# Optimization experiments

Measured on AMD Instinct MI355X. Metric: run time of the kernel, lower is better.

## Reference

```python
import jax, jax.numpy as jnp
import numpy as np

N = 50000      # nodes
E = 800000     # edges (avg degree 16)
IN = 256       # in_feats
H = 128        # hidden_feats
C = 40         # out_feats == num classes (label dim)
LPA_ITERS = 10


def setup_inputs() -> dict:
    key = jax.random.key(0)
    ks = jax.random.split(key, 9)
    features = jax.random.normal(ks[0], (N, IN), dtype=jnp.float32)
    labels = jax.random.normal(ks[1], (N, C), dtype=jnp.float32)
    mask = jax.random.randint(ks[2], (N,), 0, 2) > 0          # bool [N]
    src = jax.random.randint(ks[3], (E,), 0, N, dtype=jnp.int32)
    dst = jax.random.randint(ks[4], (E,), 0, N, dtype=jnp.int32)
    W1 = jax.random.normal(ks[5], (IN, H), dtype=jnp.float32) * (1.0 / np.sqrt(IN))
    b1 = jnp.zeros((H,), dtype=jnp.float32)
    W2 = jax.random.normal(ks[6], (H, C), dtype=jnp.float32) * (1.0 / np.sqrt(H))
    b2 = jnp.zeros((C,), dtype=jnp.float32)
    return {"features": features, "labels": labels, "mask": mask,
            "src": src, "dst": dst, "W1": W1, "b1": b1, "W2": W2, "b2": b2}


def reference(features, labels, mask, src, dst, W1, b1, W2, b2):
    ones_e = jnp.ones((E,), dtype=jnp.float32)
    deg_out = jax.ops.segment_sum(ones_e, src, num_segments=N)  # out-degree
    deg_in = jax.ops.segment_sum(ones_e, dst, num_segments=N)   # in-degree
    norm_src = jnp.maximum(deg_out, 1.0) ** -0.5                 # DGL clamps deg>=1
    norm_dst = jnp.maximum(deg_in, 1.0) ** -0.5

    def gconv(x, W, b):
        # DGL GraphConv, norm='both': D_in^{-1/2} A^T D_out^{-1/2} (x W) + b
        h = (x @ W) * norm_src[:, None]                          # [N, d_out]
        agg = jax.ops.segment_sum(h[src], dst, num_segments=N)   # gather+scatter-add
        return agg * norm_dst[:, None] + b

    x = jax.nn.relu(gconv(features, W1, b1))
    # dropout identity in eval mode
    x = gconv(x, W2, b2)

    # Label propagation: adj[src,dst]=1 so (adj @ y)[i] = sum_{(i->j)} y[j]
    masked_labels = jnp.where(mask[:, None], labels, 0.0)

    def step(y, _):
        y = jax.ops.segment_sum(y[dst], src, num_segments=N)
        y = jnp.where(mask[:, None], labels, y)
        return y, None

    y, _ = jax.lax.scan(step, masked_labels, None, length=LPA_ITERS)
    return x, y
```

## Files before the change

### kernel.cpp

```cpp
#include <hip/hip_runtime.h>

#define Nn 50000
#define Ee 800000
#define INF_ 256
#define HID 128
#define NC 40
#define CAPD 48
#define CAPS 48
#define LPA_ITERS 10
#define NB 98
#define BSH 9
#define EPB 2048
#define NBLK ((Ee + EPB - 1) / EPB)
#define CAPB_D 10240
#define CAPB_S 6144

typedef __attribute__((ext_vector_type(8))) short bfrag;
typedef __attribute__((ext_vector_type(4))) float ffrag;

__device__ inline unsigned f2bf2(float a, float b) {
    unsigned ua = __float_as_uint(a); ua += 0x7FFFu + ((ua >> 16) & 1u);
    unsigned ub = __float_as_uint(b); ub += 0x7FFFu + ((ub >> 16) & 1u);
    return (ua >> 16) | (ub & 0xFFFF0000u);
}
__device__ inline unsigned short f2bf(float a) {
    unsigned ua = __float_as_uint(a); ua += 0x7FFFu + ((ua >> 16) & 1u);
    return (unsigned short)(ua >> 16);
}
__device__ inline float bf_lo(unsigned u) { return __uint_as_float(u << 16); }
__device__ inline float bf_hi(unsigned u) { return __uint_as_float(u & 0xFFFF0000u); }

__global__ void detect_fmt(const unsigned int* __restrict__ m, int* flag) {
    int i = blockIdx.x * blockDim.x + threadIdx.x;
    if (i < 12500) {
        if (m[i] > 1u) atomicOr(flag, 1);
    }
}

__device__ inline bool read_mask(const void* mask, int node, int fmt) {
    if (fmt) return ((const unsigned char*)mask)[node] != 0;
    return ((const int*)mask)[node] != 0;
}

__global__ __launch_bounds__(256) void bin_edges(
    const int* __restrict__ src, const int* __restrict__ dst,
    const void* __restrict__ mask, const int* __restrict__ flag,
    int* __restrict__ cnt_src,
    int* __restrict__ cur_d, int* __restrict__ cur_s,
    unsigned* __restrict__ bkt_d, unsigned* __restrict__ bkt_s) {
    __shared__ unsigned stage_d[EPB];
    __shared__ unsigned stage_s[EPB];
    __shared__ int hd[NB], od[NB + 1], cd[NB], gd_[NB];
    __shared__ int hs[NB], os_[NB + 1], cs_[NB], gs_[NB];
    int tid = threadIdx.x;
    int e0 = blockIdx.x * EPB;
    int fmt = *flag;
    if (tid < NB) { hd[tid] = 0; hs[tid] = 0; }
    __syncthreads();

    int rs[EPB / 256], rd[EPB / 256];
    unsigned um = 0;
#pragma unroll
    for (int k = 0; k < EPB / 256; k++) {
        int e = e0 + tid + k * 256;
        rs[k] = -1; rd[k] = -1;
        if (e < Ee) {
            int s = src[e], d = dst[e];
            rs[k] = s; rd[k] = d;
            atomicAdd(&cnt_src[s], 1);
            atomicAdd(&hd[d >> BSH], 1);
            if (!read_mask(mask, s, fmt)) {
                um |= (1u << k);
                atomicAdd(&hs[s >> BSH], 1);
            }
        }
    }
    __syncthreads();
    if (tid == 0) {
        int run = 0;
        for (int b = 0; b < NB; b++) { od[b] = run; run += hd[b]; }
        od[NB] = run;
        run = 0;
        for (int b = 0; b < NB; b++) { os_[b] = run; run += hs[b]; }
        os_[NB] = run;
    }
    __syncthreads();
    if (tid < NB) {
        gd_[tid] = hd[tid] ? atomicAdd(&cur_d[tid], hd[tid]) : 0;
        gs_[tid] = hs[tid] ? atomicAdd(&cur_s[tid], hs[tid]) : 0;
        cd[tid] = od[tid];
        cs_[tid] = os_[tid];
    }
    __syncthreads();
#pragma unroll
    for (int k = 0; k < EPB / 256; k++) {
        if (rd[k] >= 0) {
            int p = atomicAdd(&cd[rd[k] >> BSH], 1);
            stage_d[p] = ((unsigned)rd[k] << 16) | (unsigned)rs[k];
            if (um & (1u << k)) {
                int q = atomicAdd(&cs_[rs[k] >> BSH], 1);
                stage_s[q] = ((unsigned)rs[k] << 16) | (unsigned)rd[k];
            }
        }
    }
    __syncthreads();
    int totd = od[NB];
    for (int i = tid; i < totd; i += 256) {
        int lo = 0, hi = NB;
        while (hi - lo > 1) {
            int mid = (lo + hi) >> 1;
            if (od[mid] <= i) lo = mid; else hi = mid;
        }
        int pos = gd_[lo] + (i - od[lo]);
        if (pos < CAPB_D) bkt_d[(size_t)lo * CAPB_D + pos] = stage_d[i];
    }
    int tots = os_[NB];
    for (int i = tid; i < tots; i += 256) {
        int lo = 0, hi = NB;
        while (hi - lo > 1) {
            int mid = (lo + hi) >> 1;
            if (os_[mid] <= i) lo = mid; else hi = mid;
        }
        int pos = gs_[lo] + (i - os_[lo]);
        if (pos < CAPB_S) bkt_s[(size_t)lo * CAPB_S + pos] = stage_s[i];
    }
}

__global__ __launch_bounds__(256) void build_csr_dst(
    const unsigned* __restrict__ bkt, const int* __restrict__ cur,
    int* __restrict__ adj, int* __restrict__ cnt) {
    __shared__ int lc[512];
    int b = blockIdx.x, tid = threadIdx.x;
    lc[tid] = 0; lc[tid + 256] = 0;
    __syncthreads();
    int n = cur[b]; if (n > CAPB_D) n = CAPB_D;
    int n0 = b << BSH;
    const unsigned* base = bkt + (size_t)b * CAPB_D;
    for (int i = tid; i < n; i += 256) {
        unsigned r = base[i];
        int d = r >> 16, s = r & 0xffff;
        int sl = atomicAdd(&lc[d - n0], 1);
        if (sl < CAPD) adj[d * CAPD + sl] = s;
    }
    __syncthreads();
    int g0 = n0 + tid;
    if (g0 < Nn) cnt[g0] = lc[tid];
    g0 += 256;
    if (g0 < Nn) cnt[g0] = lc[tid + 256];
}

__global__ __launch_bounds__(256) void build_csr_src(
    const unsigned* __restrict__ bkt, const int* __restrict__ cur,
    const void* __restrict__ mask, const int* __restrict__ flag,
    int* __restrict__ adj, int* __restrict__ cnt_u, int* __restrict__ cnt_m) {
    __shared__ int lu[512], lm[512];
    int b = blockIdx.x, tid = threadIdx.x;
    lu[tid] = 0; lu[tid + 256] = 0; lm[tid] = 0; lm[tid + 256] = 0;
    __syncthreads();
    int fmt = *flag;
    int n = cur[b]; if (n > CAPB_S) n = CAPB_S;
    int n0 = b << BSH;
    const unsigned* base = bkt + (size_t)b * CAPB_S;
    for (int i = tid; i < n; i += 256) {
        unsigned r = base[i];
        int s = r >> 16, d = r & 0xffff;
        if (read_mask(mask, d, fmt)) {
            int sl = atomicAdd(&lm[s - n0], 1);
            if (sl < CAPS) adj[s * CAPS + (CAPS - 1 - sl)] = d;
        } else {
            int sl = atomicAdd(&lu[s - n0], 1);
            if (sl < CAPS) adj[s * CAPS + sl] = d;
        }
    }
    __syncthreads();
    int g0 = n0 + tid;
    if (g0 < Nn) { cnt_u[g0] = lu[tid]; cnt_m[g0] = lm[tid]; }
    g0 += 256;
    if (g0 < Nn) { cnt_u[g0] = lu[tid + 256]; cnt_m[g0] = lm[tid + 256]; }
}

__global__ void build_unmasked(const void* __restrict__ mask,
                               const int* __restrict__ flag,
                               int* n_un, int* __restrict__ ulist) {
    int i = blockIdx.x * blockDim.x + threadIdx.x;
    if (i < Nn) {
        if (!read_mask(mask, i, *flag)) {
            int p = atomicAdd(n_un, 1);
            ulist[p] = i;
        }
    }
}

__global__ void prep_w1t(const float* __restrict__ W1,
                         unsigned short* __restrict__ W1t) {
    int c = blockIdx.x;
    int k = threadIdx.x;
    W1t[c * INF_ + k] = f2bf(W1[(size_t)k * HID + c]);
}

#define G1_ROWS 64
__global__ __launch_bounds__(256) void gemm1(
    const float* __restrict__ feat, const unsigned short* __restrict__ W1t,
    const int* __restrict__ cnt_src, unsigned short* __restrict__ h1b) {
    __shared__ unsigned short lA[G1_ROWS * 32];
    __shared__ unsigned short lB[HID * 32];
    const int tid = threadIdx.x;
    const int row0 = blockIdx.x * G1_ROWS;
    const int w = tid >> 6;
    const int l = tid & 63;
    const int lane15 = l & 15;
    const int quad = l >> 4;
    const int rw0 = w * 16;

    ffrag acc[8];
#pragma unroll
    for (int t = 0; t < 8; t++) acc[t] = (ffrag){0.f, 0.f, 0.f, 0.f};

    for (int k0 = 0; k0 < INF_; k0 += 32) {
#pragma unroll
        for (int p = 0; p < 2; p++) {
            int idx = tid + p * 256;
            int r = idx >> 3, c4 = idx & 7;
            int grow = row0 + r;
            float4 v = make_float4(0.f, 0.f, 0.f, 0.f);
            if (grow < Nn)
                v = *(const float4*)(feat + (size_t)grow * INF_ + k0 + c4 * 4);
            uint2 pk;
            pk.x = f2bf2(v.x, v.y);
            pk.y = f2bf2(v.z, v.w);
            *(uint2*)((char*)lA + r * 64 + c4 * 8) = pk;
        }
#pragma unroll
        for (int p = 0; p < 2; p++) {
            int idx = tid + p * 256;
            int col = idx >> 2, q = idx & 3;
            uint4 v = *(const uint4*)((const char*)W1t + col * 512 + k0 * 2 + q * 16);
            *(uint4*)((char*)lB + col * 64 + q * 16) = v;
        }
        __syncthreads();
        int arow = rw0 + lane15;
        bfrag af = *(const bfrag*)((const char*)lA + arow * 64 + quad * 16);
#pragma unroll
        for (int t = 0; t < 8; t++) {
            int col = t * 16 + lane15;
            bfrag bf = *(const bfrag*)((const char*)lB + col * 64 + quad * 16);
            acc[t] = __builtin_amdgcn_mfma_f32_16x16x32_bf16(af, bf, acc[t], 0, 0, 0);
        }
        __syncthreads();
    }
    float nrm[4];
#pragma unroll
    for (int i = 0; i < 4; i++) {
        int grow = row0 + rw0 + quad * 4 + i;
        int dg = (grow < Nn) ? cnt_src[grow] : 1;
        nrm[i] = rsqrtf((float)(dg > 1 ? dg : 1));
    }
#pragma unroll
    for (int t = 0; t < 8; t++) {
#pragma unroll
        for (int i = 0; i < 4; i++) {
            int grow = row0 + rw0 + quad * 4 + i;
            if (grow < Nn)
                h1b[(size_t)grow * HID + t * 16 + lane15] = f2bf(acc[t][i] * nrm[i]);
        }
    }
}

__global__ __launch_bounds__(256) void agg_relu1(
    const uint4* __restrict__ h1b, const int* __restrict__ adj_dst,
    const int* __restrict__ cnt_dst, const float4* __restrict__ b1,
    float4* __restrict__ x1) {
    int node = blockIdx.x * 16 + (threadIdx.x >> 4);
    int l = threadIdx.x & 15;
    int dg = cnt_dst[node];
    int cnt = dg < CAPD ? dg : CAPD;
    const int* lst = adj_dst + (size_t)node * CAPD;
    float s0 = 0.f, s1 = 0.f, s2 = 0.f, s3 = 0.f;
    float s4 = 0.f, s5 = 0.f, s6 = 0.f, s7 = 0.f;
    int e = 0;
    for (; e + 8 <= cnt; e += 8) {
        uint4 u[8];
#pragma unroll
        for (int q = 0; q < 8; q++) u[q] = h1b[(size_t)lst[e + q] * 16 + l];
#pragma unroll
        for (int q = 0; q < 8; q++) {
            s0 += bf_lo(u[q].x); s1 += bf_hi(u[q].x);
            s2 += bf_lo(u[q].y); s3 += bf_hi(u[q].y);
            s4 += bf_lo(u[q].z); s5 += bf_hi(u[q].z);
            s6 += bf_lo(u[q].w); s7 += bf_hi(u[q].w);
        }
    }
    for (; e < cnt; e++) {
        uint4 u = h1b[(size_t)lst[e] * 16 + l];
        s0 += bf_lo(u.x); s1 += bf_hi(u.x);
        s2 += bf_lo(u.y); s3 += bf_hi(u.y);
        s4 += bf_lo(u.z); s5 += bf_hi(u.z);
        s6 += bf_lo(u.w); s7 += bf_hi(u.w);
    }
    float nrm = rsqrtf((float)(dg > 1 ? dg : 1));
    float4 bb0 = b1[l * 2], bb1 = b1[l * 2 + 1];
    float4 v0, v1;
    v0.x = fmaxf(s0 * nrm + bb0.x, 0.f);
    v0.y = fmaxf(s1 * nrm + bb0.y, 0.f);
    v0.z = fmaxf(s2 * nrm + bb0.z, 0.f);
    v0.w = fmaxf(s3 * nrm + bb0.w, 0.f);
    v1.x = fmaxf(s4 * nrm + bb1.x, 0.f);
    v1.y = fmaxf(s5 * nrm + bb1.y, 0.f);
    v1.z = fmaxf(s6 * nrm + bb1.z, 0.f);
    v1.w = fmaxf(s7 * nrm + bb1.w, 0.f);
    x1[(size_t)node * 32 + l * 2] = v0;
    x1[(size_t)node * 32 + l * 2 + 1] = v1;
}

__global__ __launch_bounds__(256) void gemm2(
    const float4* __restrict__ x1, const float4* __restrict__ W2,
    const int* __restrict__ cnt_src, unsigned* __restrict__ h2b) {
    __shared__ float lw[HID * NC];
    int tid = threadIdx.x;
    for (int i = tid; i < HID * NC / 4; i += 256)
        ((float4*)lw)[i] = W2[i];
    __syncthreads();
    int r = blockIdx.x * 256 + tid;
    if (r >= Nn) return;
    const float4* xr = x1 + (size_t)r * 32;
    float4 acc[10];
#pragma unroll
    for (int j = 0; j < 10; j++) acc[j] = make_float4(0.f, 0.f, 0.f, 0.f);
    for (int k4 = 0; k4 < 32; k4++) {
        float4 xv = xr[k4];
#pragma unroll
        for (int s = 0; s < 4; s++) {
            float x = s == 0 ? xv.x : (s == 1 ? xv.y : (s == 2 ? xv.z : xv.w));
            const float4* wrow = (const float4*)(lw + (k4 * 4 + s) * NC);
#pragma unroll
            for (int j = 0; j < 10; j++) {
                float4 w = wrow[j];
                acc[j].x += x * w.x; acc[j].y += x * w.y;
                acc[j].z += x * w.z; acc[j].w += x * w.w;
            }
        }
    }
    int dg = cnt_src[r];
    float nrm = rsqrtf((float)(dg > 1 ? dg : 1));
    uint2* out = (uint2*)(h2b + (size_t)r * 20);
#pragma unroll
    for (int j = 0; j < 10; j++) {
        uint2 pk;
        pk.x = f2bf2(acc[j].x * nrm, acc[j].y * nrm);
        pk.y = f2bf2(acc[j].z * nrm, acc[j].w * nrm);
        out[j] = pk;
    }
}

__global__ __launch_bounds__(320) void agg2(
    const uint2* __restrict__ h2b, const int* __restrict__ adj_dst,
    const int* __restrict__ cnt_dst, const float4* __restrict__ b2,
    float4* __restrict__ out_x) {
    int node = blockIdx.x * 32 + threadIdx.x / 10;
    int l = threadIdx.x % 10;
    if (node >= Nn) return;
    int dg = cnt_dst[node];
    int cnt = dg < CAPD ? dg : CAPD;
    const int* lst = adj_dst + (size_t)node * CAPD;
    float s0 = 0.f, s1 = 0.f, s2 = 0.f, s3 = 0.f;
    int e = 0;
    for (; e + 8 <= cnt; e += 8) {
        uint2 u[8];
#pragma unroll
        for (int q = 0; q < 8; q++) u[q] = h2b[(size_t)lst[e + q] * 10 + l];
#pragma unroll
        for (int q = 0; q < 8; q++) {
            s0 += bf_lo(u[q].x); s1 += bf_hi(u[q].x);
            s2 += bf_lo(u[q].y); s3 += bf_hi(u[q].y);
        }
    }
    for (; e + 4 <= cnt; e += 4) {
        uint2 u[4];
#pragma unroll
        for (int q = 0; q < 4; q++) u[q] = h2b[(size_t)lst[e + q] * 10 + l];
#pragma unroll
        for (int q = 0; q < 4; q++) {
            s0 += bf_lo(u[q].x); s1 += bf_hi(u[q].x);
            s2 += bf_lo(u[q].y); s3 += bf_hi(u[q].y);
        }
    }
    for (; e < cnt; e++) {
        uint2 u = h2b[(size_t)lst[e] * 10 + l];
        s0 += bf_lo(u.x); s1 += bf_hi(u.x);
        s2 += bf_lo(u.y); s3 += bf_hi(u.y);
    }
    float nrm = rsqrtf((float)(dg > 1 ? dg : 1));
    float4 bb = b2[l];
    float4 v;
    v.x = s0 * nrm + bb.x;
    v.y = s1 * nrm + bb.y;
    v.z = s2 * nrm + bb.z;
    v.w = s3 * nrm + bb.w;
    out_x[(size_t)node * 10 + l] = v;
}

__global__ void lpa_init(const float* __restrict__ labels, const void* mask,
                         const int* __restrict__ flag, float* __restrict__ out_y) {
    int g = blockIdx.x * blockDim.x + threadIdx.x;
    if (g >= Nn * NC) return;
    int node = g / NC;
    if (read_mask(mask, node, *flag)) out_y[g] = labels[g];
}

__global__ __launch_bounds__(320) void lpa_const(
    const float4* __restrict__ labels, const int* __restrict__ n_un,
    const int* __restrict__ ulist, const int* __restrict__ adj_s,
    const int* __restrict__ cnt_m, float4* __restrict__ sconst,
    uint2* __restrict__ y1b) {
    int g = blockIdx.x * 32 + threadIdx.x / 10;
    int l = threadIdx.x % 10;
    if (g >= *n_un) return;
    int u = ulist[g];
    int cm = cnt_m[u];
    int cnt = cm < CAPS ? cm : CAPS;
    const int* lst = adj_s + (size_t)u * CAPS + (CAPS - cnt);
    float4 s = make_float4(0.f, 0.f, 0.f, 0.f);
    int e = 0;
    for (; e + 8 <= cnt; e += 8) {
        float4 v[8];
#pragma unroll
        for (int q = 0; q < 8; q++) v[q] = labels[(size_t)lst[e + q] * 10 + l];
#pragma unroll
        for (int q = 0; q < 8; q++) {
            s.x += v[q].x; s.y += v[q].y; s.z += v[q].z; s.w += v[q].w;
        }
    }
    for (; e + 4 <= cnt; e += 4) {
        float4 v[4];
#pragma unroll
        for (int q = 0; q < 4; q++) v[q] = labels[(size_t)lst[e + q] * 10 + l];
#pragma unroll
        for (int q = 0; q < 4; q++) {
            s.x += v[q].x; s.y += v[q].y; s.z += v[q].z; s.w += v[q].w;
        }
    }
    for (; e < cnt; e++) {
        float4 a = labels[(size_t)lst[e] * 10 + l];
        s.x += a.x; s.y += a.y; s.z += a.z; s.w += a.w;
    }
    sconst[(size_t)u * 10 + l] = s;
    uint2 pk; pk.x = f2bf2(s.x, s.y); pk.y = f2bf2(s.z, s.w);
    y1b[(size_t)u * 10 + l] = pk;
}

__global__ __launch_bounds__(320) void lpa_mid(
    const uint2* __restrict__ ycur, const int* __restrict__ n_un,
    const int* __restrict__ ulist, const int* __restrict__ adj_s,
    const int* __restrict__ cnt_u, const float4* __restrict__ sconst,
    uint2* __restrict__ ynext) {
    int g = blockIdx.x * 32 + threadIdx.x / 10;
    int l = threadIdx.x % 10;
    if (g >= *n_un) return;
    int u = ulist[g];
    int cu = cnt_u[u];
    int cnt = cu < CAPS ? cu : CAPS;
    const int* lst = adj_s + (size_t)u * CAPS;
    float4 s = sconst[(size_t)u * 10 + l];
    int e = 0;
    for (; e + 8 <= cnt; e += 8) {
        uint2 v[8];
#pragma unroll
        for (int q = 0; q < 8; q++) v[q] = ycur[(size_t)lst[e + q] * 10 + l];
#pragma unroll
        for (int q = 0; q < 8; q++) {
            s.x += bf_lo(v[q].x); s.y += bf_hi(v[q].x);
            s.z += bf_lo(v[q].y); s.w += bf_hi(v[q].y);
        }
    }
    for (; e + 4 <= cnt; e += 4) {
        uint2 v[4];
#pragma unroll
        for (int q = 0; q < 4; q++) v[q] = ycur[(size_t)lst[e + q] * 10 + l];
#pragma unroll
        for (int q = 0; q < 4; q++) {
            s.x += bf_lo(v[q].x); s.y += bf_hi(v[q].x);
            s.z += bf_lo(v[q].y); s.w += bf_hi(v[q].y);
        }
    }
    for (; e < cnt; e++) {
        uint2 v = ycur[(size_t)lst[e] * 10 + l];
        s.x += bf_lo(v.x); s.y += bf_hi(v.x);
        s.z += bf_lo(v.y); s.w += bf_hi(v.y);
    }
    uint2 pk; pk.x = f2bf2(s.x, s.y); pk.y = f2bf2(s.z, s.w);
    ynext[(size_t)u * 10 + l] = pk;
}

__global__ __launch_bounds__(320) void lpa_last(
    const uint2* __restrict__ ycur, const int* __restrict__ n_un,
    const int* __restrict__ ulist, const int* __restrict__ adj_s,
    const int* __restrict__ cnt_u, const float4* __restrict__ sconst,
    float4* __restrict__ out_y) {
    int g = blockIdx.x * 32 + threadIdx.x / 10;
    int l = threadIdx.x % 10;
    if (g >= *n_un) return;
    int u = ulist[g];
    int cu = cnt_u[u];
    int cnt = cu < CAPS ? cu : CAPS;
    const int* lst = adj_s + (size_t)u * CAPS;
    float4 s = sconst[(size_t)u * 10 + l];
    int e = 0;
    for (; e + 8 <= cnt; e += 8) {
        uint2 v[8];
#pragma unroll
        for (int q = 0; q < 8; q++) v[q] = ycur[(size_t)lst[e + q] * 10 + l];
#pragma unroll
        for (int q = 0; q < 8; q++) {
            s.x += bf_lo(v[q].x); s.y += bf_hi(v[q].x);
            s.z += bf_lo(v[q].y); s.w += bf_hi(v[q].y);
        }
    }
    for (; e + 4 <= cnt; e += 4) {
        uint2 v[4];
#pragma unroll
        for (int q = 0; q < 4; q++) v[q] = ycur[(size_t)lst[e + q] * 10 + l];
#pragma unroll
        for (int q = 0; q < 4; q++) {
            s.x += bf_lo(v[q].x); s.y += bf_hi(v[q].x);
            s.z += bf_lo(v[q].y); s.w += bf_hi(v[q].y);
        }
    }
    for (; e < cnt; e++) {
        uint2 v = ycur[(size_t)lst[e] * 10 + l];
        s.x += bf_lo(v.x); s.y += bf_hi(v.x);
        s.z += bf_lo(v.y); s.w += bf_hi(v.y);
    }
    out_y[(size_t)u * 10 + l] = s;
}

extern "C" void kernel_launch(void* const* d_in, const int* in_sizes, int n_in,
                              void* d_out, int out_size, void* d_ws, size_t ws_size,
                              hipStream_t stream) {
    const float* feat   = (const float*)d_in[0];
    const float* labels = (const float*)d_in[1];
    const void*  mask   = d_in[2];
    const int*   src    = (const int*)d_in[3];
    const int*   dst    = (const int*)d_in[4];
    const float* W1     = (const float*)d_in[5];
    const float* b1     = (const float*)d_in[6];
    const float* W2     = (const float*)d_in[7];
    const float* b2     = (const float*)d_in[8];

    float* out_x = (float*)d_out;
    float* out_y = out_x + (size_t)Nn * NC;

    char* ws = (char*)d_ws;
    size_t off = 0;
    auto alloc = [&](size_t bytes) -> void* {
        void* p = ws + off;
        off += (bytes + 255) & ~(size_t)255;
        return p;
    };
    int* flag    = (int*)alloc(256);
    int* n_un    = flag + 1;
    int* cnt_src = (int*)alloc((size_t)Nn * 4);
    int* cur_d   = (int*)alloc(512);
    int* cur_s   = (int*)alloc(512);
    size_t zero_bytes = off;
    int* cnt_dst = (int*)alloc((size_t)Nn * 4);
    int* cnt_u   = (int*)alloc((size_t)Nn * 4);
    int* cnt_m   = (int*)alloc((size_t)Nn * 4);
    int* ulist   = (int*)alloc((size_t)Nn * 4);
    unsigned short* W1t = (unsigned short*)alloc((size_t)HID * INF_ * 2);
    char* uni = (char*)alloc((size_t)Nn * HID * 2);
    unsigned* bkt_d = (unsigned*)uni;
    unsigned* bkt_s = (unsigned*)(uni + (size_t)NB * CAPB_D * 4);
    unsigned short* h1b = (unsigned short*)uni;
    float* x1 = (float*)alloc((size_t)Nn * HID * 4);
    int* adj_s   = (int*)alloc((size_t)Nn * CAPS * 4);
    int* adj_dst = (int*)alloc((size_t)Nn * CAPD * 4);
    unsigned* h2b = (unsigned*)alloc((size_t)Nn * NC * 2);
    float* sconst = (float*)alloc((size_t)Nn * NC * 4);
    uint2* y1b = (uint2*)alloc((size_t)Nn * NC * 2);
    uint2* y2b = (uint2*)alloc((size_t)Nn * NC * 2);

    hipMemsetAsync(d_ws, 0, zero_bytes, stream);

    detect_fmt<<<49, 256, 0, stream>>>((const unsigned int*)mask, flag);
    prep_w1t<<<HID, INF_, 0, stream>>>(W1, W1t);
    bin_edges<<<NBLK, 256, 0, stream>>>(src, dst, mask, flag, cnt_src,
                                        cur_d, cur_s, bkt_d, bkt_s);
    build_csr_dst<<<NB, 256, 0, stream>>>(bkt_d, cur_d, adj_dst, cnt_dst);
    build_csr_src<<<NB, 256, 0, stream>>>(bkt_s, cur_s, mask, flag,
                                          adj_s, cnt_u, cnt_m);
    build_unmasked<<<196, 256, 0, stream>>>(mask, flag, n_un, ulist);

    gemm1<<<(Nn + G1_ROWS - 1) / G1_ROWS, 256, 0, stream>>>(feat, W1t, cnt_src, h1b);
    agg_relu1<<<Nn / 16, 256, 0, stream>>>((const uint4*)h1b, adj_dst, cnt_dst,
                                           (const float4*)b1, (float4*)x1);
    gemm2<<<196, 256, 0, stream>>>((const float4*)x1, (const float4*)W2,
                                   cnt_src, h2b);
    agg2<<<(Nn + 31) / 32, 320, 0, stream>>>((const uint2*)h2b, adj_dst, cnt_dst,
                                             (const float4*)b2, (float4*)out_x);

    lpa_init<<<(Nn * NC + 255) / 256, 256, 0, stream>>>(labels, mask, flag, out_y);
    lpa_const<<<(Nn + 31) / 32, 320, 0, stream>>>(
        (const float4*)labels, n_un, ulist, adj_s, cnt_m, (float4*)sconst, y1b);
    const uint2* cur = y1b;
    for (int i = 0; i < 8; i++) {
        uint2* nxt = (i & 1) ? y1b : y2b;
        lpa_mid<<<(Nn + 31) / 32, 320, 0, stream>>>(
            cur, n_un, ulist, adj_s, cnt_u, (const float4*)sconst, nxt);
        cur = nxt;
    }
    lpa_last<<<(Nn + 31) / 32, 320, 0, stream>>>(
        cur, n_un, ulist, adj_s, cnt_u, (const float4*)sconst, (float4*)out_y);
}
```

Baseline: 398.2 us.

## Merge CSR build kernels, parallelize bin prefix scan, halve edges per block

Fuses the two CSR-building kernels into one launch of 2*NB blocks so dst and src bucket processing run concurrently instead of back to back. The serial single-thread prefix sum over 98 bins in bin_edges is replaced by a parallel Hillis-Steele scan across 256 threads. EPB is halved to 1024, which doubles the number of binning blocks for more parallelism but also doubles the global atomics on the per-bucket cursors. The scan adds 14 barriers per block.

```diff
diff --git a/kernel.cpp b/kernel.cpp
--- a/kernel.cpp
+++ b/kernel.cpp
@@ -10,7 +10,7 @@
 #define LPA_ITERS 10
 #define NB 98
 #define BSH 9
-#define EPB 2048
+#define EPB 1024
 #define NBLK ((Ee + EPB - 1) / EPB)
 #define CAPB_D 10240
 #define CAPB_S 6144
@@ -52,6 +52,7 @@
     __shared__ unsigned stage_s[EPB];
     __shared__ int hd[NB], od[NB + 1], cd[NB], gd_[NB];
     __shared__ int hs[NB], os_[NB + 1], cs_[NB], gs_[NB];
+    __shared__ int sc[256];
     int tid = threadIdx.x;
     int e0 = blockIdx.x * EPB;
     int fmt = *flag;
@@ -76,13 +77,27 @@
         }
     }
     __syncthreads();
-    if (tid == 0) {
-        int run = 0;
-        for (int b = 0; b < NB; b++) { od[b] = run; run += hd[b]; }
-        od[NB] = run;
-        run = 0;
-        for (int b = 0; b < NB; b++) { os_[b] = run; run += hs[b]; }
-        os_[NB] = run;
+    {
+        int seg = tid >> 7;
+        int i = tid & 127;
+        int v = 0;
+        if (i < NB) v = seg ? hs[i] : hd[i];
+        sc[tid] = v;
+        __syncthreads();
+#pragma unroll
+        for (int offs = 1; offs < 128; offs <<= 1) {
+            int add = (i >= offs) ? sc[tid - offs] : 0;
+            __syncthreads();
+            sc[tid] += add;
+            __syncthreads();
+        }
+        if (i < NB) {
+            int excl = i ? sc[tid - 1] : 0;
+            if (seg == 0) od[i] = excl; else os_[i] = excl;
+            if (i == NB - 1) {
+                if (seg == 0) od[NB] = sc[tid]; else os_[NB] = sc[tid];
+            }
+        }
     }
     __syncthreads();
     if (tid < NB) {
@@ -126,57 +141,55 @@
     }
 }
 
-__global__ __launch_bounds__(256) void build_csr_dst(
-    const unsigned* __restrict__ bkt, const int* __restrict__ cur,
-    int* __restrict__ adj, int* __restrict__ cnt) {
-    __shared__ int lc[512];
-    int b = blockIdx.x, tid = threadIdx.x;
-    lc[tid] = 0; lc[tid + 256] = 0;
-    __syncthreads();
-    int n = cur[b]; if (n > CAPB_D) n = CAPB_D;
-    int n0 = b << BSH;
-    const unsigned* base = bkt + (size_t)b * CAPB_D;
-    for (int i = tid; i < n; i += 256) {
-        unsigned r = base[i];
-        int d = r >> 16, s = r & 0xffff;
-        int sl = atomicAdd(&lc[d - n0], 1);
-        if (sl < CAPD) adj[d * CAPD + sl] = s;
-    }
-    __syncthreads();
-    int g0 = n0 + tid;
-    if (g0 < Nn) cnt[g0] = lc[tid];
-    g0 += 256;
-    if (g0 < Nn) cnt[g0] = lc[tid + 256];
-}
-
-__global__ __launch_bounds__(256) void build_csr_src(
-    const unsigned* __restrict__ bkt, const int* __restrict__ cur,
+__global__ __launch_bounds__(256) void build_csr_both(
+    const unsigned* __restrict__ bkt_d, const int* __restrict__ cur_d,
+    const unsigned* __restrict__ bkt_s, const int* __restrict__ cur_s,
     const void* __restrict__ mask, const int* __restrict__ flag,
-    int* __restrict__ adj, int* __restrict__ cnt_u, int* __restrict__ cnt_m) {
+    int* __restrict__ adj_dst, int* __restrict__ cnt_dst,
+    int* __restrict__ adj_s, int* __restrict__ cnt_u, int* __restrict__ cnt_m) {
     __shared__ int lu[512], lm[512];
-    int b = blockIdx.x, tid = threadIdx.x;
+    int bb = blockIdx.x, tid = threadIdx.x;
     lu[tid] = 0; lu[tid + 256] = 0; lm[tid] = 0; lm[tid + 256] = 0;
     __syncthreads();
-    int fmt = *flag;
-    int n = cur[b]; if (n > CAPB_S) n = CAPB_S;
-    int n0 = b << BSH;
-    const unsigned* base = bkt + (size_t)b * CAPB_S;
-    for (int i = tid; i < n; i += 256) {
-        unsigned r = base[i];
-        int s = r >> 16, d = r & 0xffff;
-        if (read_mask(mask, d, fmt)) {
-            int sl = atomicAdd(&lm[s - n0], 1);
-            if (sl < CAPS) adj[s * CAPS + (CAPS - 1 - sl)] = d;
-        } else {
-            int sl = atomicAdd(&lu[s - n0], 1);
-            if (sl < CAPS) adj[s * CAPS + sl] = d;
-        }
-    }
-    __syncthreads();
-    int g0 = n0 + tid;
-    if (g0 < Nn) { cnt_u[g0] = lu[tid]; cnt_m[g0] = lm[tid]; }
-    g0 += 256;
-    if (g0 < Nn) { cnt_u[g0] = lu[tid + 256]; cnt_m[g0] = lm[tid + 256]; }
+    if (bb < NB) {
+        int b = bb;
+        int n = cur_d[b]; if (n > CAPB_D) n = CAPB_D;
+        int n0 = b << BSH;
+        const unsigned* base = bkt_d + (size_t)b * CAPB_D;
+        for (int i = tid; i < n; i += 256) {
+            unsigned r = base[i];
+            int d = r >> 16, s = r & 0xffff;
+            int sl = atomicAdd(&lu[d - n0], 1);
+            if (sl < CAPD) adj_dst[d * CAPD + sl] = s;
+        }
+        __syncthreads();
+        int g0 = n0 + tid;
+        if (g0 < Nn) cnt_dst[g0] = lu[tid];
+        g0 += 256;
+        if (g0 < Nn) cnt_dst[g0] = lu[tid + 256];
+    } else {
+        int b = bb - NB;
+        int fmt = *flag;
+        int n = cur_s[b]; if (n > CAPB_S) n = CAPB_S;
+        int n0 = b << BSH;
+        const unsigned* base = bkt_s + (size_t)b * CAPB_S;
+        for (int i = tid; i < n; i += 256) {
+            unsigned r = base[i];
+            int s = r >> 16, d = r & 0xffff;
+            if (read_mask(mask, d, fmt)) {
+                int sl = atomicAdd(&lm[s - n0], 1);
+                if (sl < CAPS) adj_s[s * CAPS + (CAPS - 1 - sl)] = d;
+            } else {
+                int sl = atomicAdd(&lu[s - n0], 1);
+                if (sl < CAPS) adj_s[s * CAPS + sl] = d;
+            }
+        }
+        __syncthreads();
+        int g0 = n0 + tid;
+        if (g0 < Nn) { cnt_u[g0] = lu[tid]; cnt_m[g0] = lm[tid]; }
+        g0 += 256;
+        if (g0 < Nn) { cnt_u[g0] = lu[tid + 256]; cnt_m[g0] = lm[tid + 256]; }
+    }
 }
 
 __global__ void build_unmasked(const void* __restrict__ mask,
@@ -585,9 +598,9 @@
     prep_w1t<<<HID, INF_, 0, stream>>>(W1, W1t);
     bin_edges<<<NBLK, 256, 0, stream>>>(src, dst, mask, flag, cnt_src,
                                         cur_d, cur_s, bkt_d, bkt_s);
-    build_csr_dst<<<NB, 256, 0, stream>>>(bkt_d, cur_d, adj_dst, cnt_dst);
-    build_csr_src<<<NB, 256, 0, stream>>>(bkt_s, cur_s, mask, flag,
-                                          adj_s, cnt_u, cnt_m);
+    build_csr_both<<<NB * 2, 256, 0, stream>>>(bkt_d, cur_d, bkt_s, cur_s,
+                                               mask, flag, adj_dst, cnt_dst,
+                                               adj_s, cnt_u, cnt_m);
     build_unmasked<<<196, 256, 0, stream>>>(mask, flag, n_un, ulist);
 
     gemm1<<<(Nn + G1_ROWS - 1) / G1_ROWS, 256, 0, stream>>>(feat, W1t, cnt_src, h1b);
```

Result: faster. 390.2 us (-2.0%).
